# Kernel optimization log

Measured on AMD Instinct MI355X. Metric: run time of the kernel, lower is better.

## Reference

```python
import jax, jax.numpy as jnp
import numpy as np

B, S = 64, 1024
D_INPUT, D_POLAR, N_LAYERS, KAN, N_CLASSES = 256, 256, 8, 32, 1000
PI = float(np.pi)
EPS = 1e-8


def _gelu(v):
    return jax.nn.gelu(v, approximate=False)  # torch nn.GELU default = exact erf


def setup_inputs() -> dict:
    key = jax.random.key(0)
    ks = jax.random.split(key, 16)

    def rn(k, shape, fan_in):
        return jax.random.normal(k, shape, jnp.float32) / np.sqrt(fan_in)

    return {
        "x": jax.random.normal(ks[0], (B, S, D_INPUT), jnp.float32),
        "embed_w": rn(ks[1], (D_INPUT, 2 * D_POLAR), D_INPUT),
        "embed_b": jnp.zeros((2 * D_POLAR,), jnp.float32),
        "mag_w1": rn(ks[2], (N_LAYERS, 1, KAN), 1),
        "mag_b1": jnp.zeros((N_LAYERS, KAN), jnp.float32),
        "mag_w2": rn(ks[3], (N_LAYERS, KAN, 1), KAN),
        "mag_b2": jnp.zeros((N_LAYERS, 1), jnp.float32),
        "ph_w1": rn(ks[4], (N_LAYERS, 2, KAN), 2),
        "ph_b1": jnp.zeros((N_LAYERS, KAN), jnp.float32),
        "ph_w2": rn(ks[5], (N_LAYERS, KAN, 2), KAN),
        "ph_b2": jnp.zeros((N_LAYERS, 2), jnp.float32),
        "cls_w1": rn(ks[6], (D_POLAR, KAN), D_POLAR),
        "cls_b1": jnp.zeros((KAN,), jnp.float32),
        "cls_w2": rn(ks[7], (KAN, N_CLASSES), KAN),
        "cls_b2": jnp.zeros((N_CLASSES,), jnp.float32),
    }


def _forward(x, embed_w, embed_b, mag_w1, mag_b1, mag_w2, mag_b2,
             ph_w1, ph_b1, ph_w2, ph_b2, cls_w1, cls_b1, cls_w2, cls_b2):
    h = x @ embed_w + embed_b                      # [B,S,2D]
    r = jnp.abs(h[..., :D_POLAR]) + 0.1            # [B,S,D]
    theta = h[..., D_POLAR:] * PI                  # [B,S,D]
    for i in range(N_LAYERS):
        xc = r * jnp.cos(theta)
        yc = r * jnp.sin(theta)
        xm = xc.mean(axis=1, keepdims=True)        # [B,1,D]
        ym = yc.mean(axis=1, keepdims=True)
        r_agg = jnp.sqrt(xm * xm + ym * ym + EPS)
        th_agg = jnp.arctan2(ym, xm)
        # magnitude MLP (1 -> 32 -> 1) in log space, per channel
        log_r = jnp.log(r_agg + EPS)[..., None]    # [B,1,D,1]
        lr = _gelu(log_r @ mag_w1[i] + mag_b1[i]) @ mag_w2[i] + mag_b2[i]
        r_trans = jnp.exp(lr[..., 0])              # [B,1,D]
        # phase MLP (2 -> 32 -> 2) on (sin, cos)
        pin = jnp.stack([jnp.sin(th_agg), jnp.cos(th_agg)], axis=-1)  # [B,1,D,2]
        pout = _gelu(pin @ ph_w1[i] + ph_b1[i]) @ ph_w2[i] + ph_b2[i]
        norm = jnp.sqrt(pout[..., 0] ** 2 + pout[..., 1] ** 2 + EPS)
        th_trans = jnp.arctan2(pout[..., 0] / norm, pout[..., 1] / norm)
        x_out = xc + r_trans * jnp.cos(th_trans)
        y_out = yc + r_trans * jnp.sin(th_trans)
        r = jnp.sqrt(x_out * x_out + y_out * y_out + EPS)
        theta = jnp.arctan2(y_out, x_out)
    pooled = r.mean(axis=1)                        # [B,D]
    return _gelu(pooled @ cls_w1 + cls_b1) @ cls_w2 + cls_b2  # [B,n_classes]


def reference(x, embed_w, embed_b, mag_w1, mag_b1, mag_w2, mag_b2,
              ph_w1, ph_b1, ph_w2, ph_b2, cls_w1, cls_b1, cls_w2, cls_b2):
    return _forward(x, embed_w, embed_b, mag_w1, mag_b1, mag_w2, mag_b2,
                    ph_w1, ph_b1, ph_w2, ph_b2, cls_w1, cls_b1, cls_w2, cls_b2)
```

## Files before the change

### kernel.cpp

```cpp
#include <hip/hip_runtime.h>
#include <hip/hip_bf16.h>
#include <hip/hip_fp16.h>

#define EPS 1e-8f
#define PI_F 3.14159265358979323846f

typedef _Float16 half8 __attribute__((ext_vector_type(8)));
typedef float f32x4 __attribute__((ext_vector_type(4)));
typedef float f32x2 __attribute__((ext_vector_type(2)));

__device__ __forceinline__ float gelu_exact(float v) {
    return 0.5f * v * (1.0f + erff(v * 0.70710678118654752f));
}

__global__ void convertW(const float* __restrict__ W,
                         _Float16* __restrict__ Wth, _Float16* __restrict__ Wtl,
                         float* __restrict__ zero_base) {
    int idx = blockIdx.x * 256 + threadIdx.x;
    if (idx < 49152) zero_base[idx] = 0.f;
    int col = idx & 511, k = idx >> 9;
    int d  = col & 255;
    int g  = d >> 6;
    int dl = d & 63;
    int r  = (dl >> 5) * 64 + ((col >> 8) << 5) + (dl & 31);
    int kt = k >> 5, ko = k & 31;
    float f = W[k * 512 + col];
    _Float16 h = (_Float16)f;
    int o = ((g * 8 + kt) * 128 + r) * 32 + ko;
    Wth[o] = h;
    Wtl[o] = (_Float16)(f - (float)h);
}

__global__ __launch_bounds__(256, 4) void gemm_embed(
    const float* __restrict__ x,
    const _Float16* __restrict__ Wth, const _Float16* __restrict__ Wtl,
    const float* __restrict__ bias,
    unsigned short* __restrict__ XY8,
    float* __restrict__ XMsum, float* __restrict__ YMsum)
{
    __shared__ __attribute__((aligned(16))) _Float16 Ah[4096], Al[4096];
    const int tid  = threadIdx.x;
    const int wave = tid >> 6;
    const int lane = tid & 63;
    const int wm   = wave >> 1;
    const int wn   = wave & 1;
    const int id   = blockIdx.x;
    const int xcd  = id & 7;
    const int s    = id >> 3;
    const int g    = s & 3;
    const int mt   = (s >> 2) * 8 + xcd;
    const int m0   = mt * 128;
    const int q    = lane >> 4, ln = lane & 15;

    f32x4 acc[4][4];
#pragma unroll
    for (int mi = 0; mi < 4; ++mi)
#pragma unroll
        for (int nt = 0; nt < 4; ++nt)
            acc[mi][nt] = (f32x4){0.f, 0.f, 0.f, 0.f};

    for (int kt = 0; kt < 8; ++kt) {
        half8 bh[4], bl[4];
        {
            const int tbase = (g * 8 + kt) * 4096;
#pragma unroll
            for (int nt = 0; nt < 4; ++nt) {
                int off = tbase + (wn * 64 + nt * 16 + ln) * 32 + q * 8;
                bh[nt] = *(const half8*)(Wth + off);
                bl[nt] = *(const half8*)(Wtl + off);
            }
        }
        __syncthreads();
#pragma unroll
        for (int L = 0; L < 2; ++L) {
            int idx2 = L * 256 + tid;
            int r = idx2 >> 2, cq = idx2 & 3;
            const float* src = x + (size_t)(m0 + r) * 256 + kt * 32 + cq * 8;
            const float4 f0 = *(const float4*)(src);
            const float4 f1 = *(const float4*)(src + 4);
            half8 hh, ll;
            hh[0] = (_Float16)f0.x; ll[0] = (_Float16)(f0.x - (float)hh[0]);
            hh[1] = (_Float16)f0.y; ll[1] = (_Float16)(f0.y - (float)hh[1]);
            hh[2] = (_Float16)f0.z; ll[2] = (_Float16)(f0.z - (float)hh[2]);
            hh[3] = (_Float16)f0.w; ll[3] = (_Float16)(f0.w - (float)hh[3]);
            hh[4] = (_Float16)f1.x; ll[4] = (_Float16)(f1.x - (float)hh[4]);
            hh[5] = (_Float16)f1.y; ll[5] = (_Float16)(f1.y - (float)hh[5]);
            hh[6] = (_Float16)f1.z; ll[6] = (_Float16)(f1.z - (float)hh[6]);
            hh[7] = (_Float16)f1.w; ll[7] = (_Float16)(f1.w - (float)hh[7]);
            int pos = cq ^ ((r >> 1) & 3);
            *(half8*)&Ah[r * 32 + pos * 8] = hh;
            *(half8*)&Al[r * 32 + pos * 8] = ll;
        }
        __syncthreads();

        half8 am[4];
#pragma unroll
        for (int mi = 0; mi < 4; ++mi) {
            int row = wm * 64 + mi * 16 + ln;
            am[mi] = *(const half8*)&Ah[row * 32 + (q ^ ((row >> 1) & 3)) * 8];
        }
#pragma unroll
        for (int mi = 0; mi < 4; ++mi)
#pragma unroll
            for (int nt = 0; nt < 4; ++nt)
                acc[mi][nt] = __builtin_amdgcn_mfma_f32_16x16x32_f16(am[mi], bh[nt], acc[mi][nt], 0, 0, 0);
#pragma unroll
        for (int mi = 0; mi < 4; ++mi)
#pragma unroll
            for (int nt = 0; nt < 4; ++nt)
                acc[mi][nt] = __builtin_amdgcn_mfma_f32_16x16x32_f16(am[mi], bl[nt], acc[mi][nt], 0, 0, 0);
#pragma unroll
        for (int mi = 0; mi < 4; ++mi) {
            int row = wm * 64 + mi * 16 + ln;
            half8 alv = *(const half8*)&Al[row * 32 + (q ^ ((row >> 1) & 3)) * 8];
#pragma unroll
            for (int nt = 0; nt < 4; ++nt)
                acc[mi][nt] = __builtin_amdgcn_mfma_f32_16x16x32_f16(alv, bh[nt], acc[mi][nt], 0, 0, 0);
        }
    }

    const int d0 = g * 64 + wn * 32 + ln;
    const int d1 = d0 + 16;
    const int b  = m0 >> 10;
    const float b1_0 = bias[d0],       b1_1 = bias[d1];
    const float b2_0 = bias[256 + d0], b2_1 = bias[256 + d1];
    float sx0 = 0.f, sy0 = 0.f, sx1 = 0.f, sy1 = 0.f;
#pragma unroll
    for (int mi = 0; mi < 4; ++mi) {
#pragma unroll
        for (int i = 0; i < 4; ++i) {
            const int row = m0 + wm * 64 + mi * 16 + q * 4 + i;
            {
                const float h1 = acc[mi][0][i] + b1_0;
                const float h2 = acc[mi][2][i] + b2_0;
                const float rr = fabsf(h1) + 0.1f;
                float sv, cv;
                __sincosf(PI_F * h2, &sv, &cv);
                const float xc = rr * cv, yc = rr * sv;
                int pk = __builtin_amdgcn_cvt_pk_fp8_f32(xc, yc, 0, false);
                XY8[(size_t)row * 256 + d0] = (unsigned short)pk;
                sx0 += xc; sy0 += yc;
            }
            {
                const float h1 = acc[mi][1][i] + b1_1;
                const float h2 = acc[mi][3][i] + b2_1;
                const float rr = fabsf(h1) + 0.1f;
                float sv, cv;
                __sincosf(PI_F * h2, &sv, &cv);
                const float xc = rr * cv, yc = rr * sv;
                int pk = __builtin_amdgcn_cvt_pk_fp8_f32(xc, yc, 0, false);
                XY8[(size_t)row * 256 + d1] = (unsigned short)pk;
                sx1 += xc; sy1 += yc;
            }
        }
    }
    sx0 += __shfl_down(sx0, 32); sx0 += __shfl_down(sx0, 16);
    sy0 += __shfl_down(sy0, 32); sy0 += __shfl_down(sy0, 16);
    sx1 += __shfl_down(sx1, 32); sx1 += __shfl_down(sx1, 16);
    sy1 += __shfl_down(sy1, 32); sy1 += __shfl_down(sy1, 16);
    if (lane < 16) {
        atomicAdd(&XMsum[b * 256 + d0], sx0);
        atomicAdd(&YMsum[b * 256 + d0], sy0);
        atomicAdd(&XMsum[b * 256 + d1], sx1);
        atomicAdd(&YMsum[b * 256 + d1], sy1);
    }
}

__global__ __launch_bounds__(256) void tail_kernel(
    const float* __restrict__ XMsum, const float* __restrict__ YMsum,
    const float* __restrict__ mw1, const float* __restrict__ mb1,
    const float* __restrict__ mw2, const float* __restrict__ mb2,
    const float* __restrict__ pw1, const float* __restrict__ pb1,
    const float* __restrict__ pw2, const float* __restrict__ pb2,
    const unsigned short* __restrict__ XY8,
    float* __restrict__ pooled)
{
    __shared__ float s_mw1[256], s_mb1[256], s_mw2[256], s_mb2[8];
    __shared__ float s_pw1[512], s_pb1[256], s_pw2[512], s_pb2[16];
    __shared__ float dxl[64], dyl[64];
    __shared__ float red[256][9];
    const int b = blockIdx.x, qd = blockIdx.y, tid = threadIdx.x;

    s_mw1[tid] = mw1[tid]; s_mb1[tid] = mb1[tid];
    s_mw2[tid] = mw2[tid]; s_pb1[tid] = pb1[tid];
    s_pw1[tid] = pw1[tid]; s_pw1[256 + tid] = pw1[256 + tid];
    s_pw2[tid] = pw2[tid]; s_pw2[256 + tid] = pw2[256 + tid];
    if (tid < 8)  s_mb2[tid] = mb2[tid];
    if (tid < 16) s_pb2[tid] = pb2[tid];
    __syncthreads();

#pragma unroll 1
    for (int it = 0; it < 2; ++it) {
        const int u    = it * 256 + tid;
        const int sub  = u & 7;
        const int dloc = u >> 3;
        const int idx  = b * 256 + qd * 64 + dloc;
        float xm = XMsum[idx] * (1.0f / 1024.0f);
        float ym = YMsum[idx] * (1.0f / 1024.0f);
        float dxa = 0.f, dya = 0.f;
#pragma unroll 1
        for (int i = 0; i < 8; ++i) {
            float r2    = xm * xm + ym * ym;
            float r_agg = sqrtf(r2 + EPS);
            float hyp   = sqrtf(r2);
            float inv   = hyp > 0.f ? 1.0f / hyp : 0.f;
            float st    = ym * inv;
            float ct    = hyp > 0.f ? xm * inv : 1.0f;
            float log_r = logf(r_agg + EPS);
            float lr = 0.f, p0 = 0.f, p1 = 0.f;
#pragma unroll
            for (int k4 = 0; k4 < 4; ++k4) {
                int k = sub * 4 + k4;
                float hm = gelu_exact(log_r * s_mw1[i * 32 + k] + s_mb1[i * 32 + k]);
                lr += hm * s_mw2[i * 32 + k];
                float hp = gelu_exact(st * s_pw1[i * 64 + k] + ct * s_pw1[i * 64 + 32 + k] + s_pb1[i * 32 + k]);
                p0 += hp * s_pw2[i * 64 + 2 * k + 0];
                p1 += hp * s_pw2[i * 64 + 2 * k + 1];
            }
            lr += __shfl_xor(lr, 1); lr += __shfl_xor(lr, 2); lr += __shfl_xor(lr, 4);
            p0 += __shfl_xor(p0, 1); p0 += __shfl_xor(p0, 2); p0 += __shfl_xor(p0, 4);
            p1 += __shfl_xor(p1, 1); p1 += __shfl_xor(p1, 2); p1 += __shfl_xor(p1, 4);
            lr += s_mb2[i];
            p0 += s_pb2[i * 2 + 0];
            p1 += s_pb2[i * 2 + 1];
            float r_trans = expf(lr);
            float hp2  = sqrtf(p0 * p0 + p1 * p1);
            float invp = hp2 > 0.f ? 1.0f / hp2 : 0.f;
            float ctt  = hp2 > 0.f ? p1 * invp : 1.0f;
            float stt  = p0 * invp;
            float dx = r_trans * ctt;
            float dy = r_trans * stt;
            dxa += dx; dya += dy; xm += dx; ym += dy;
        }
        if (sub == 0) { dxl[dloc] = dxa; dyl[dloc] = dya; }
    }
    __syncthreads();

    {
        const int dg = tid & 7;
        const int sh = tid >> 3;
        const int d0 = qd * 64 + dg * 8;
        float dxv[8], dyv[8], sacc[8];
#pragma unroll
        for (int j = 0; j < 8; ++j) {
            dxv[j] = dxl[dg * 8 + j];
            dyv[j] = dyl[dg * 8 + j];
            sacc[j] = 0.f;
        }
        const size_t base = ((size_t)b * 1024 + sh * 32) * 256 + d0;
#pragma unroll 4
        for (int i = 0; i < 32; ++i) {
            const int4 v = *(const int4*)(XY8 + base + (size_t)i * 256);
            const int wv[4] = {v.x, v.y, v.z, v.w};
#pragma unroll
            for (int w = 0; w < 4; ++w) {
                f32x2 pa = __builtin_amdgcn_cvt_pk_f32_fp8(wv[w], false);
                f32x2 pb = __builtin_amdgcn_cvt_pk_f32_fp8(wv[w], true);
                float xa = pa[0] + dxv[2 * w],     ya = pa[1] + dyv[2 * w];
                float xb = pb[0] + dxv[2 * w + 1], yb = pb[1] + dyv[2 * w + 1];
                sacc[2 * w]     += sqrtf(xa * xa + ya * ya + EPS);
                sacc[2 * w + 1] += sqrtf(xb * xb + yb * yb + EPS);
            }
        }
#pragma unroll
        for (int j = 0; j < 8; ++j) red[tid][j] = sacc[j];
    }
    __syncthreads();
    if (tid < 64) {
        const int dgq = tid >> 3, j = tid & 7;
        float t = 0.f;
#pragma unroll
        for (int c = 0; c < 32; ++c) t += red[c * 8 + dgq][j];
        pooled[b * 256 + qd * 64 + dgq * 8 + j] = t;
    }
}

__global__ __launch_bounds__(256) void cls_kernel(
    const float* __restrict__ pooled,
    const float* __restrict__ w1, const float* __restrict__ b1,
    const float* __restrict__ w2, const float* __restrict__ b2,
    float* __restrict__ out)
{
    __shared__ float pl[256];
    __shared__ float part[8][32];
    __shared__ float hd[32];
    const int b = blockIdx.x, yc = blockIdx.y, tid = threadIdx.x;
    pl[tid] = pooled[b * 256 + tid] * (1.0f / 1024.0f);
    __syncthreads();
    const int hu = tid & 31, kc = tid >> 5;
    float a = 0.f;
    for (int k = kc * 32; k < kc * 32 + 32; ++k) a += pl[k] * w1[k * 32 + hu];
    part[kc][hu] = a;
    __syncthreads();
    if (tid < 32) {
        float s = b1[tid];
#pragma unroll
        for (int c = 0; c < 8; ++c) s += part[c][tid];
        hd[tid] = gelu_exact(s);
    }
    __syncthreads();
    const int n0 = yc * 250;
    const int nend = (n0 + 250 < 1000) ? n0 + 250 : 1000;
    for (int n = n0 + tid; n < nend; n += 256) {
        float s = b2[n];
#pragma unroll
        for (int k = 0; k < 32; ++k) s += hd[k] * w2[k * 1000 + n];
        out[b * 1000 + n] = s;
    }
}

extern "C" void kernel_launch(void* const* d_in, const int* in_sizes, int n_in,
                              void* d_out, int out_size, void* d_ws, size_t ws_size,
                              hipStream_t stream)
{
    const float* x       = (const float*)d_in[0];
    const float* embed_w = (const float*)d_in[1];
    const float* embed_b = (const float*)d_in[2];
    const float* mag_w1  = (const float*)d_in[3];
    const float* mag_b1  = (const float*)d_in[4];
    const float* mag_w2  = (const float*)d_in[5];
    const float* mag_b2  = (const float*)d_in[6];
    const float* ph_w1   = (const float*)d_in[7];
    const float* ph_b1   = (const float*)d_in[8];
    const float* ph_w2   = (const float*)d_in[9];
    const float* ph_b2   = (const float*)d_in[10];
    const float* cls_w1  = (const float*)d_in[11];
    const float* cls_b1  = (const float*)d_in[12];
    const float* cls_w2  = (const float*)d_in[13];
    const float* cls_b2  = (const float*)d_in[14];
    float* out = (float*)d_out;

    char* ws = (char*)d_ws;
    unsigned short* XY8 = (unsigned short*)(ws + 0);
    _Float16* Wth = (_Float16*)(ws + 33554432);
    _Float16* Wtl = (_Float16*)(ws + 33816576);
    float* XMsum  = (float*)(ws + 34078720);
    float* YMsum  = (float*)(ws + 34144256);
    float* pooled = (float*)(ws + 34209792);

    convertW<<<512, 256, 0, stream>>>(embed_w, Wth, Wtl, XMsum);
    gemm_embed<<<2048, 256, 0, stream>>>(x, Wth, Wtl, embed_b, XY8, XMsum, YMsum);
    tail_kernel<<<dim3(64, 4), 256, 0, stream>>>(XMsum, YMsum,
                                                 mag_w1, mag_b1, mag_w2, mag_b2,
                                                 ph_w1, ph_b1, ph_w2, ph_b2,
                                                 XY8, pooled);
    cls_kernel<<<dim3(64, 4), 256, 0, stream>>>(pooled, cls_w1, cls_b1, cls_w2, cls_b2, out);
}
```

Measured before the change: 209.1 us.

## Fuse weight split into GEMM, replace atomics with partial sums, widen tail grid

New measurement: 205.1 us. About the same (-1.9%).

```diff
diff --git a/kernel.cpp b/kernel.cpp
--- a/kernel.cpp
+++ b/kernel.cpp
@@ -13,30 +13,12 @@
     return 0.5f * v * (1.0f + erff(v * 0.70710678118654752f));
 }
 
-__global__ void convertW(const float* __restrict__ W,
-                         _Float16* __restrict__ Wth, _Float16* __restrict__ Wtl,
-                         float* __restrict__ zero_base) {
-    int idx = blockIdx.x * 256 + threadIdx.x;
-    if (idx < 49152) zero_base[idx] = 0.f;
-    int col = idx & 511, k = idx >> 9;
-    int d  = col & 255;
-    int g  = d >> 6;
-    int dl = d & 63;
-    int r  = (dl >> 5) * 64 + ((col >> 8) << 5) + (dl & 31);
-    int kt = k >> 5, ko = k & 31;
-    float f = W[k * 512 + col];
-    _Float16 h = (_Float16)f;
-    int o = ((g * 8 + kt) * 128 + r) * 32 + ko;
-    Wth[o] = h;
-    Wtl[o] = (_Float16)(f - (float)h);
-}
-
 __global__ __launch_bounds__(256, 4) void gemm_embed(
     const float* __restrict__ x,
-    const _Float16* __restrict__ Wth, const _Float16* __restrict__ Wtl,
+    const float* __restrict__ W,
     const float* __restrict__ bias,
     unsigned short* __restrict__ XY8,
-    float* __restrict__ XMsum, float* __restrict__ YMsum)
+    float* __restrict__ XMpart, float* __restrict__ YMpart)
 {
     __shared__ __attribute__((aligned(16))) _Float16 Ah[4096], Al[4096];
     const int tid  = threadIdx.x;
@@ -52,6 +34,13 @@
     const int m0   = mt * 128;
     const int q    = lane >> 4, ln = lane & 15;
 
+    const int d0 = g * 64 + wn * 32 + ln;
+    const int d1 = d0 + 16;
+    const float* wc0 = W + d0;
+    const float* wc1 = W + d1;
+    const float* wc2 = W + 256 + d0;
+    const float* wc3 = W + 256 + d1;
+
     f32x4 acc[4][4];
 #pragma unroll
     for (int mi = 0; mi < 4; ++mi)
@@ -60,17 +49,16 @@
             acc[mi][nt] = (f32x4){0.f, 0.f, 0.f, 0.f};
 
     for (int kt = 0; kt < 8; ++kt) {
-        half8 bh[4], bl[4];
-        {
-            const int tbase = (g * 8 + kt) * 4096;
-#pragma unroll
-            for (int nt = 0; nt < 4; ++nt) {
-                int off = tbase + (wn * 64 + nt * 16 + ln) * 32 + q * 8;
-                bh[nt] = *(const half8*)(Wth + off);
-                bl[nt] = *(const half8*)(Wtl + off);
-            }
-        }
         __syncthreads();
+        float wf0[8], wf1[8], wf2[8], wf3[8];
+#pragma unroll
+        for (int j = 0; j < 8; ++j) {
+            const int ko = (kt * 32 + q * 8 + j) * 512;
+            wf0[j] = wc0[ko];
+            wf1[j] = wc1[ko];
+            wf2[j] = wc2[ko];
+            wf3[j] = wc3[ko];
+        }
 #pragma unroll
         for (int L = 0; L < 2; ++L) {
             int idx2 = L * 256 + tid;
@@ -93,6 +81,19 @@
         }
         __syncthreads();
 
+        half8 bh[4], bl[4];
+#pragma unroll
+        for (int j = 0; j < 8; ++j) {
+            _Float16 h0 = (_Float16)wf0[j];
+            bh[0][j] = h0; bl[0][j] = (_Float16)(wf0[j] - (float)h0);
+            _Float16 h1v = (_Float16)wf1[j];
+            bh[1][j] = h1v; bl[1][j] = (_Float16)(wf1[j] - (float)h1v);
+            _Float16 h2v = (_Float16)wf2[j];
+            bh[2][j] = h2v; bl[2][j] = (_Float16)(wf2[j] - (float)h2v);
+            _Float16 h3v = (_Float16)wf3[j];
+            bh[3][j] = h3v; bl[3][j] = (_Float16)(wf3[j] - (float)h3v);
+        }
+
         half8 am[4];
 #pragma unroll
         for (int mi = 0; mi < 4; ++mi) {
@@ -119,9 +120,6 @@
         }
     }
 
-    const int d0 = g * 64 + wn * 32 + ln;
-    const int d1 = d0 + 16;
-    const int b  = m0 >> 10;
     const float b1_0 = bias[d0],       b1_1 = bias[d1];
     const float b2_0 = bias[256 + d0], b2_1 = bias[256 + d1];
     float sx0 = 0.f, sy0 = 0.f, sx1 = 0.f, sy1 = 0.f;
@@ -158,16 +156,26 @@
     sy0 += __shfl_down(sy0, 32); sy0 += __shfl_down(sy0, 16);
     sx1 += __shfl_down(sx1, 32); sx1 += __shfl_down(sx1, 16);
     sy1 += __shfl_down(sy1, 32); sy1 += __shfl_down(sy1, 16);
-    if (lane < 16) {
-        atomicAdd(&XMsum[b * 256 + d0], sx0);
-        atomicAdd(&YMsum[b * 256 + d0], sy0);
-        atomicAdd(&XMsum[b * 256 + d1], sx1);
-        atomicAdd(&YMsum[b * 256 + d1], sy1);
+
+    __syncthreads();
+    float* sc = (float*)Ah;
+    if (wm == 0 && lane < 16) {
+        sc[wn * 64 + ln]            = sx0;
+        sc[wn * 64 + 16 + ln]       = sx1;
+        sc[128 + wn * 64 + ln]      = sy0;
+        sc[128 + wn * 64 + 16 + ln] = sy1;
+    }
+    __syncthreads();
+    if (wm == 1 && lane < 16) {
+        XMpart[mt * 256 + d0] = sx0 + sc[wn * 64 + ln];
+        XMpart[mt * 256 + d1] = sx1 + sc[wn * 64 + 16 + ln];
+        YMpart[mt * 256 + d0] = sy0 + sc[128 + wn * 64 + ln];
+        YMpart[mt * 256 + d1] = sy1 + sc[128 + wn * 64 + 16 + ln];
     }
 }
 
 __global__ __launch_bounds__(256) void tail_kernel(
-    const float* __restrict__ XMsum, const float* __restrict__ YMsum,
+    const float* __restrict__ XMpart, const float* __restrict__ YMpart,
     const float* __restrict__ mw1, const float* __restrict__ mb1,
     const float* __restrict__ mw2, const float* __restrict__ mb2,
     const float* __restrict__ pw1, const float* __restrict__ pb1,
@@ -177,9 +185,9 @@
 {
     __shared__ float s_mw1[256], s_mb1[256], s_mw2[256], s_mb2[8];
     __shared__ float s_pw1[512], s_pb1[256], s_pw2[512], s_pb2[16];
-    __shared__ float dxl[64], dyl[64];
+    __shared__ float dxl[32], dyl[32];
     __shared__ float red[256][9];
-    const int b = blockIdx.x, qd = blockIdx.y, tid = threadIdx.x;
+    const int b = blockIdx.x, q8 = blockIdx.y, tid = threadIdx.x;
 
     s_mw1[tid] = mw1[tid]; s_mb1[tid] = mb1[tid];
     s_mw2[tid] = mw2[tid]; s_pb1[tid] = pb1[tid];
@@ -189,14 +197,16 @@
     if (tid < 16) s_pb2[tid] = pb2[tid];
     __syncthreads();
 
-#pragma unroll 1
-    for (int it = 0; it < 2; ++it) {
-        const int u    = it * 256 + tid;
-        const int sub  = u & 7;
-        const int dloc = u >> 3;
-        const int idx  = b * 256 + qd * 64 + dloc;
-        float xm = XMsum[idx] * (1.0f / 1024.0f);
-        float ym = YMsum[idx] * (1.0f / 1024.0f);
+    {
+        const int sub  = tid & 7;
+        const int dloc = tid >> 3;
+        const int d    = q8 * 32 + dloc;
+        float xm = XMpart[(b * 8 + sub) * 256 + d];
+        float ym = YMpart[(b * 8 + sub) * 256 + d];
+        xm += __shfl_xor(xm, 1); xm += __shfl_xor(xm, 2); xm += __shfl_xor(xm, 4);
+        ym += __shfl_xor(ym, 1); ym += __shfl_xor(ym, 2); ym += __shfl_xor(ym, 4);
+        xm *= (1.0f / 1024.0f);
+        ym *= (1.0f / 1024.0f);
         float dxa = 0.f, dya = 0.f;
 #pragma unroll 1
         for (int i = 0; i < 8; ++i) {
@@ -237,9 +247,9 @@
     __syncthreads();
 
     {
-        const int dg = tid & 7;
-        const int sh = tid >> 3;
-        const int d0 = qd * 64 + dg * 8;
+        const int dg = tid & 3;
+        const int sh = tid >> 2;
+        const int d0 = q8 * 32 + dg * 8;
         float dxv[8], dyv[8], sacc[8];
 #pragma unroll
         for (int j = 0; j < 8; ++j) {
@@ -247,9 +257,9 @@
             dyv[j] = dyl[dg * 8 + j];
             sacc[j] = 0.f;
         }
-        const size_t base = ((size_t)b * 1024 + sh * 32) * 256 + d0;
+        const size_t base = ((size_t)b * 1024 + sh * 16) * 256 + d0;
 #pragma unroll 4
-        for (int i = 0; i < 32; ++i) {
+        for (int i = 0; i < 16; ++i) {
             const int4 v = *(const int4*)(XY8 + base + (size_t)i * 256);
             const int wv[4] = {v.x, v.y, v.z, v.w};
 #pragma unroll
@@ -266,12 +276,12 @@
         for (int j = 0; j < 8; ++j) red[tid][j] = sacc[j];
     }
     __syncthreads();
-    if (tid < 64) {
+    if (tid < 32) {
         const int dgq = tid >> 3, j = tid & 7;
         float t = 0.f;
 #pragma unroll
-        for (int c = 0; c < 32; ++c) t += red[c * 8 + dgq][j];
-        pooled[b * 256 + qd * 64 + dgq * 8 + j] = t;
+        for (int c = 0; c < 64; ++c) t += red[c * 4 + dgq][j];
+        pooled[b * 256 + q8 * 32 + dgq * 8 + j] = t;
     }
 }
 
@@ -332,15 +342,12 @@
 
     char* ws = (char*)d_ws;
     unsigned short* XY8 = (unsigned short*)(ws + 0);
-    _Float16* Wth = (_Float16*)(ws + 33554432);
-    _Float16* Wtl = (_Float16*)(ws + 33816576);
-    float* XMsum  = (float*)(ws + 34078720);
-    float* YMsum  = (float*)(ws + 34144256);
-    float* pooled = (float*)(ws + 34209792);
-
-    convertW<<<512, 256, 0, stream>>>(embed_w, Wth, Wtl, XMsum);
-    gemm_embed<<<2048, 256, 0, stream>>>(x, Wth, Wtl, embed_b, XY8, XMsum, YMsum);
-    tail_kernel<<<dim3(64, 4), 256, 0, stream>>>(XMsum, YMsum,
+    float* XMpart = (float*)(ws + 33554432);
+    float* YMpart = (float*)(ws + 34078720);
+    float* pooled = (float*)(ws + 34603008);
+
+    gemm_embed<<<2048, 256, 0, stream>>>(x, embed_w, embed_b, XY8, XMpart, YMpart);
+    tail_kernel<<<dim3(64, 8), 256, 0, stream>>>(XMpart, YMpart,
                                                  mag_w1, mag_b1, mag_w2, mag_b2,
                                                  ph_w1, ph_b1, ph_w2, ph_b2,
                                                  XY8, pooled);
```

## Stage two K-tiles per barrier in embed GEMM and double tail kernel grid

Applied to the files above, without the earlier changes.

Result: slower. 245.8 us (+17.5%).

```diff
diff --git a/kernel.cpp b/kernel.cpp
--- a/kernel.cpp
+++ b/kernel.cpp
@@ -38,7 +38,7 @@
     unsigned short* __restrict__ XY8,
     float* __restrict__ XMsum, float* __restrict__ YMsum)
 {
-    __shared__ __attribute__((aligned(16))) _Float16 Ah[4096], Al[4096];
+    __shared__ __attribute__((aligned(16))) _Float16 Ah[8192], Al[8192];
     const int tid  = threadIdx.x;
     const int wave = tid >> 6;
     const int lane = tid & 63;
@@ -59,63 +59,103 @@
         for (int nt = 0; nt < 4; ++nt)
             acc[mi][nt] = (f32x4){0.f, 0.f, 0.f, 0.f};
 
-    for (int kt = 0; kt < 8; ++kt) {
-        half8 bh[4], bl[4];
+#pragma unroll 1
+    for (int kp = 0; kp < 4; ++kp) {
+        half8 bh0[4], bl0[4];
         {
-            const int tbase = (g * 8 + kt) * 4096;
+            const int tbase = (g * 8 + 2 * kp) * 4096;
 #pragma unroll
             for (int nt = 0; nt < 4; ++nt) {
                 int off = tbase + (wn * 64 + nt * 16 + ln) * 32 + q * 8;
-                bh[nt] = *(const half8*)(Wth + off);
-                bl[nt] = *(const half8*)(Wtl + off);
+                bh0[nt] = *(const half8*)(Wth + off);
+                bl0[nt] = *(const half8*)(Wtl + off);
             }
         }
         __syncthreads();
 #pragma unroll
-        for (int L = 0; L < 2; ++L) {
-            int idx2 = L * 256 + tid;
-            int r = idx2 >> 2, cq = idx2 & 3;
-            const float* src = x + (size_t)(m0 + r) * 256 + kt * 32 + cq * 8;
-            const float4 f0 = *(const float4*)(src);
-            const float4 f1 = *(const float4*)(src + 4);
-            half8 hh, ll;
-            hh[0] = (_Float16)f0.x; ll[0] = (_Float16)(f0.x - (float)hh[0]);
-            hh[1] = (_Float16)f0.y; ll[1] = (_Float16)(f0.y - (float)hh[1]);
-            hh[2] = (_Float16)f0.z; ll[2] = (_Float16)(f0.z - (float)hh[2]);
-            hh[3] = (_Float16)f0.w; ll[3] = (_Float16)(f0.w - (float)hh[3]);
-            hh[4] = (_Float16)f1.x; ll[4] = (_Float16)(f1.x - (float)hh[4]);
-            hh[5] = (_Float16)f1.y; ll[5] = (_Float16)(f1.y - (float)hh[5]);
-            hh[6] = (_Float16)f1.z; ll[6] = (_Float16)(f1.z - (float)hh[6]);
-            hh[7] = (_Float16)f1.w; ll[7] = (_Float16)(f1.w - (float)hh[7]);
-            int pos = cq ^ ((r >> 1) & 3);
-            *(half8*)&Ah[r * 32 + pos * 8] = hh;
-            *(half8*)&Al[r * 32 + pos * 8] = ll;
+        for (int h = 0; h < 2; ++h) {
+#pragma unroll
+            for (int L = 0; L < 2; ++L) {
+                int idx2 = L * 256 + tid;
+                int r = idx2 >> 2, cq = idx2 & 3;
+                const float* src = x + (size_t)(m0 + r) * 256 + (2 * kp + h) * 32 + cq * 8;
+                const float4 f0 = *(const float4*)(src);
+                const float4 f1 = *(const float4*)(src + 4);
+                half8 hh, ll;
+                hh[0] = (_Float16)f0.x; ll[0] = (_Float16)(f0.x - (float)hh[0]);
+                hh[1] = (_Float16)f0.y; ll[1] = (_Float16)(f0.y - (float)hh[1]);
+                hh[2] = (_Float16)f0.z; ll[2] = (_Float16)(f0.z - (float)hh[2]);
+                hh[3] = (_Float16)f0.w; ll[3] = (_Float16)(f0.w - (float)hh[3]);
+                hh[4] = (_Float16)f1.x; ll[4] = (_Float16)(f1.x - (float)hh[4]);
+                hh[5] = (_Float16)f1.y; ll[5] = (_Float16)(f1.y - (float)hh[5]);
+                hh[6] = (_Float16)f1.z; ll[6] = (_Float16)(f1.z - (float)hh[6]);
+                hh[7] = (_Float16)f1.w; ll[7] = (_Float16)(f1.w - (float)hh[7]);
+                int pos = cq ^ ((r >> 1) & 3);
+                *(half8*)&Ah[h * 4096 + r * 32 + pos * 8] = hh;
+                *(half8*)&Al[h * 4096 + r * 32 + pos * 8] = ll;
+            }
         }
         __syncthreads();
 
-        half8 am[4];
-#pragma unroll
-        for (int mi = 0; mi < 4; ++mi) {
-            int row = wm * 64 + mi * 16 + ln;
-            am[mi] = *(const half8*)&Ah[row * 32 + (q ^ ((row >> 1) & 3)) * 8];
-        }
-#pragma unroll
-        for (int mi = 0; mi < 4; ++mi)
-#pragma unroll
-            for (int nt = 0; nt < 4; ++nt)
-                acc[mi][nt] = __builtin_amdgcn_mfma_f32_16x16x32_f16(am[mi], bh[nt], acc[mi][nt], 0, 0, 0);
-#pragma unroll
-        for (int mi = 0; mi < 4; ++mi)
-#pragma unroll
-            for (int nt = 0; nt < 4; ++nt)
-                acc[mi][nt] = __builtin_amdgcn_mfma_f32_16x16x32_f16(am[mi], bl[nt], acc[mi][nt], 0, 0, 0);
-#pragma unroll
-        for (int mi = 0; mi < 4; ++mi) {
-            int row = wm * 64 + mi * 16 + ln;
-            half8 alv = *(const half8*)&Al[row * 32 + (q ^ ((row >> 1) & 3)) * 8];
-#pragma unroll
-            for (int nt = 0; nt < 4; ++nt)
-                acc[mi][nt] = __builtin_amdgcn_mfma_f32_16x16x32_f16(alv, bh[nt], acc[mi][nt], 0, 0, 0);
+        {
+            half8 am[4];
+#pragma unroll
+            for (int mi = 0; mi < 4; ++mi) {
+                int row = wm * 64 + mi * 16 + ln;
+                am[mi] = *(const half8*)&Ah[row * 32 + (q ^ ((row >> 1) & 3)) * 8];
+            }
+#pragma unroll
+            for (int mi = 0; mi < 4; ++mi)
+#pragma unroll
+                for (int nt = 0; nt < 4; ++nt)
+                    acc[mi][nt] = __builtin_amdgcn_mfma_f32_16x16x32_f16(am[mi], bh0[nt], acc[mi][nt], 0, 0, 0);
+#pragma unroll
+            for (int mi = 0; mi < 4; ++mi)
+#pragma unroll
+                for (int nt = 0; nt < 4; ++nt)
+                    acc[mi][nt] = __builtin_amdgcn_mfma_f32_16x16x32_f16(am[mi], bl0[nt], acc[mi][nt], 0, 0, 0);
+#pragma unroll
+            for (int mi = 0; mi < 4; ++mi) {
+                int row = wm * 64 + mi * 16 + ln;
+                half8 alv = *(const half8*)&Al[row * 32 + (q ^ ((row >> 1) & 3)) * 8];
+#pragma unroll
+                for (int nt = 0; nt < 4; ++nt)
+                    acc[mi][nt] = __builtin_amdgcn_mfma_f32_16x16x32_f16(alv, bh0[nt], acc[mi][nt], 0, 0, 0);
+            }
+        }
+        {
+            half8 bh1[4], bl1[4];
+            const int tbase = (g * 8 + 2 * kp + 1) * 4096;
+#pragma unroll
+            for (int nt = 0; nt < 4; ++nt) {
+                int off = tbase + (wn * 64 + nt * 16 + ln) * 32 + q * 8;
+                bh1[nt] = *(const half8*)(Wth + off);
+                bl1[nt] = *(const half8*)(Wtl + off);
+            }
+            half8 am[4];
+#pragma unroll
+            for (int mi = 0; mi < 4; ++mi) {
+                int row = wm * 64 + mi * 16 + ln;
+                am[mi] = *(const half8*)&Ah[4096 + row * 32 + (q ^ ((row >> 1) & 3)) * 8];
+            }
+#pragma unroll
+            for (int mi = 0; mi < 4; ++mi)
+#pragma unroll
+                for (int nt = 0; nt < 4; ++nt)
+                    acc[mi][nt] = __builtin_amdgcn_mfma_f32_16x16x32_f16(am[mi], bh1[nt], acc[mi][nt], 0, 0, 0);
+#pragma unroll
+            for (int mi = 0; mi < 4; ++mi)
+#pragma unroll
+                for (int nt = 0; nt < 4; ++nt)
+                    acc[mi][nt] = __builtin_amdgcn_mfma_f32_16x16x32_f16(am[mi], bl1[nt], acc[mi][nt], 0, 0, 0);
+#pragma unroll
+            for (int mi = 0; mi < 4; ++mi) {
+                int row = wm * 64 + mi * 16 + ln;
+                half8 alv = *(const half8*)&Al[4096 + row * 32 + (q ^ ((row >> 1) & 3)) * 8];
+#pragma unroll
+                for (int nt = 0; nt < 4; ++nt)
+                    acc[mi][nt] = __builtin_amdgcn_mfma_f32_16x16x32_f16(alv, bh1[nt], acc[mi][nt], 0, 0, 0);
+            }
         }
     }
 
@@ -177,9 +217,9 @@
 {
     __shared__ float s_mw1[256], s_mb1[256], s_mw2[256], s_mb2[8];
     __shared__ float s_pw1[512], s_pb1[256], s_pw2[512], s_pb2[16];
-    __shared__ float dxl[64], dyl[64];
+    __shared__ float dxl[32], dyl[32];
     __shared__ float red[256][9];
-    const int b = blockIdx.x, qd = blockIdx.y, tid = threadIdx.x;
+    const int b = blockIdx.x, q8 = blockIdx.y, tid = threadIdx.x;
 
     s_mw1[tid] = mw1[tid]; s_mb1[tid] = mb1[tid];
     s_mw2[tid] = mw2[tid]; s_pb1[tid] = pb1[tid];
@@ -189,12 +229,10 @@
     if (tid < 16) s_pb2[tid] = pb2[tid];
     __syncthreads();
 
-#pragma unroll 1
-    for (int it = 0; it < 2; ++it) {
-        const int u    = it * 256 + tid;
-        const int sub  = u & 7;
-        const int dloc = u >> 3;
-        const int idx  = b * 256 + qd * 64 + dloc;
+    {
+        const int sub  = tid & 7;
+        const int dloc = tid >> 3;
+        const int idx  = b * 256 + q8 * 32 + dloc;
         float xm = XMsum[idx] * (1.0f / 1024.0f);
         float ym = YMsum[idx] * (1.0f / 1024.0f);
         float dxa = 0.f, dya = 0.f;
@@ -237,9 +275,9 @@
     __syncthreads();
 
     {
-        const int dg = tid & 7;
-        const int sh = tid >> 3;
-        const int d0 = qd * 64 + dg * 8;
+        const int dg = tid & 3;
+        const int sh = tid >> 2;
+        const int d0 = q8 * 32 + dg * 8;
         float dxv[8], dyv[8], sacc[8];
 #pragma unroll
         for (int j = 0; j < 8; ++j) {
@@ -247,9 +285,9 @@
             dyv[j] = dyl[dg * 8 + j];
             sacc[j] = 0.f;
         }
-        const size_t base = ((size_t)b * 1024 + sh * 32) * 256 + d0;
+        const size_t base = ((size_t)b * 1024 + sh * 16) * 256 + d0;
 #pragma unroll 4
-        for (int i = 0; i < 32; ++i) {
+        for (int i = 0; i < 16; ++i) {
             const int4 v = *(const int4*)(XY8 + base + (size_t)i * 256);
             const int wv[4] = {v.x, v.y, v.z, v.w};
 #pragma unroll
@@ -266,12 +304,12 @@
         for (int j = 0; j < 8; ++j) red[tid][j] = sacc[j];
     }
     __syncthreads();
-    if (tid < 64) {
+    if (tid < 32) {
         const int dgq = tid >> 3, j = tid & 7;
         float t = 0.f;
 #pragma unroll
-        for (int c = 0; c < 32; ++c) t += red[c * 8 + dgq][j];
-        pooled[b * 256 + qd * 64 + dgq * 8 + j] = t;
+        for (int c = 0; c < 64; ++c) t += red[c * 4 + dgq][j];
+        pooled[b * 256 + q8 * 32 + dgq * 8 + j] = t;
     }
 }
 
@@ -340,7 +378,7 @@
 
     convertW<<<512, 256, 0, stream>>>(embed_w, Wth, Wtl, XMsum);
     gemm_embed<<<2048, 256, 0, stream>>>(x, Wth, Wtl, embed_b, XY8, XMsum, YMsum);
-    tail_kernel<<<dim3(64, 4), 256, 0, stream>>>(XMsum, YMsum,
+    tail_kernel<<<dim3(64, 8), 256, 0, stream>>>(XMsum, YMsum,
                                                  mag_w1, mag_b1, mag_w2, mag_b2,
                                                  ph_w1, ph_b1, ph_w2, ph_b2,
                                                  XY8, pooled);
```
